# Performance work log

Measured on AMD Instinct MI355X. Metric: run time of the kernel, lower is better.

The kernel has to match this reference:

```python
import jax, jax.numpy as jnp
import numpy as np

B, S, H = 8, 2048, 256
MAX_SEQ = 2048


def get_rotary_matrix(context_window, embedding_dim):
    # Faithful to the llama-from-scratch construction (note the (i-1) quirk):
    # theta_i = 10000 ** (-2*(i-1)/d) for i in [0, d/2)
    half = embedding_dim // 2
    i = jnp.arange(half, dtype=jnp.float32)
    theta = jnp.power(10000.0, -2.0 * (i - 1.0) / embedding_dim)  # [half]
    pos = jnp.arange(context_window, dtype=jnp.float32)  # [S]
    ang = pos[:, None] * theta[None, :]  # [S, half]
    c, s = jnp.cos(ang), jnp.sin(ang)
    R = jnp.zeros((context_window, embedding_dim, embedding_dim), dtype=jnp.float32)
    idx = jnp.arange(half)
    R = R.at[:, 2 * idx, 2 * idx].set(c)
    R = R.at[:, 2 * idx, 2 * idx + 1].set(-s)
    R = R.at[:, 2 * idx + 1, 2 * idx].set(s)
    R = R.at[:, 2 * idx + 1, 2 * idx + 1].set(c)
    return R


def setup_inputs() -> dict:
    key = jax.random.key(0)
    kx, kq, kk, kv = jax.random.split(key, 4)
    scale = 1.0 / np.sqrt(H)
    x = jax.random.normal(kx, (B, S, H), dtype=jnp.float32)
    wq = jax.random.uniform(kq, (H, H), dtype=jnp.float32, minval=-scale, maxval=scale)
    wk = jax.random.uniform(kk, (H, H), dtype=jnp.float32, minval=-scale, maxval=scale)
    wv = jax.random.uniform(kv, (H, H), dtype=jnp.float32, minval=-scale, maxval=scale)
    r = get_rotary_matrix(MAX_SEQ, H)
    return {"x": x, "wq": wq, "wk": wk, "wv": wv, "r": r}


def reference(x, wq, wk, wv, r):
    b, s, h = x.shape
    # nn.Linear(bias=False): y = x @ W.T
    q = jnp.einsum("bsh,oh->bso", x, wq)
    k = jnp.einsum("bsh,oh->bso", x, wk)
    v = jnp.einsum("bsh,oh->bso", x, wv)
    # per-position dense rotary rotation: qr[b,s,:] = q[b,s,:] @ r[s]
    rs = r[:s]
    qr = jnp.einsum("bsh,shk->bsk", q, rs)
    kr = jnp.einsum("bsh,shk->bsk", k, rs)
    attn = jnp.einsum("bqh,bkh->bqk", qr, kr) * (h ** -0.5)  # [B,S,S]
    causal = jnp.tril(jnp.ones((s, s), dtype=bool))
    attn = jnp.where(causal[None, :, :], attn, -jnp.inf)
    attn = jax.nn.softmax(attn, axis=-1)
    out = jnp.einsum("bqk,bkh->bqh", attn, v)
    return out
```

## Files before the change

### kernel.cpp

```cpp
#include <hip/hip_runtime.h>


typedef __bf16 bf16x8 __attribute__((ext_vector_type(8)));
typedef float  f32x4  __attribute__((ext_vector_type(4)));
typedef unsigned short u16x4 __attribute__((ext_vector_type(4)));

#define LOG2E 1.44269504088896340736f
#define LOG2_10000 13.287712379549449f

__device__ __forceinline__ unsigned short f2bf(float f) {
    union { __bf16 h; unsigned short u; } cv;
    cv.h = (__bf16)f;
    return cv.u;
}

__device__ __forceinline__ void gl_lds16(const unsigned short* g, unsigned short* lds) {
    __builtin_amdgcn_global_load_lds(
        (const __attribute__((address_space(1))) unsigned int*)g,
        (__attribute__((address_space(3))) unsigned int*)lds, 16, 0, 0);
}

__global__ __launch_bounds__(256) void prep(
    const float* __restrict__ wq, const float* __restrict__ wk,
    const float* __restrict__ wv,
    float2* __restrict__ cs, unsigned short* __restrict__ wb) {
    int bid = blockIdx.x;
    if (bid < 1024) {
        int id = bid * 256 + threadIdx.x;
        int s = id >> 7;
        int i = id & 127;
        float ex = -2.0f * ((float)i - 1.0f) * (1.0f / 256.0f);
        float theta = exp2f(LOG2_10000 * ex);
        float ang = (float)s * theta;
        float sn, c;
        sincosf(ang, &sn, &c);
        cs[id] = make_float2(c, sn);
    } else {
        int id = (bid - 1024) * 256 + threadIdx.x;
        int sel = id >> 14;
        int off = id & 16383;
        const float* src = (sel == 0) ? wq : (sel == 1) ? wk : wv;
        float4 d = ((const float4*)src)[off];
        u16x4 pk = { f2bf(d.x), f2bf(d.y), f2bf(d.z), f2bf(d.w) };
        *(u16x4*)&wb[(size_t)sel * 65536 + (size_t)off * 4] = pk;
    }
}

__global__ __launch_bounds__(256, 2) void qkv_rope(
    const float* __restrict__ x, const unsigned short* __restrict__ wb,
    const float2* __restrict__ cs,
    unsigned short* __restrict__ qr, unsigned short* __restrict__ kr,
    unsigned short* __restrict__ vt) {

    __shared__ unsigned short Ash[32 * 256];
    __shared__ unsigned short Bsh[256 * 128];

    const int mt  = blockIdx.x;
    const int tid = threadIdx.x;
    const int w = tid >> 6, l = tid & 63;
    const int lane_m = l & 15, quad = l >> 4;
    const int wm = w >> 1, wn = w & 1;

#pragma unroll
    for (int p = 0; p < 8; ++p) {
        int id = p * 256 + tid;
        int row = id >> 6, f4 = id & 63;
        float4 d = *(const float4*)(x + (size_t)(mt * 32 + row) * 256 + f4 * 4);
        u16x4 pk = { f2bf(d.x), f2bf(d.y), f2bf(d.z), f2bf(d.w) };
        int k = f4 * 4;
        int idx = row * 256 + ((((k >> 3) ^ row) << 3) | (k & 7));
        *(u16x4*)&Ash[idx] = pk;
    }

    for (int sel = 0; sel < 3; ++sel) {
        f32x4 acc[8];
#pragma unroll
        for (int c = 0; c < 8; ++c) acc[c] = (f32x4){0.f, 0.f, 0.f, 0.f};

        for (int kc2 = 0; kc2 < 2; ++kc2) {
            __syncthreads();
#pragma unroll
            for (int p = 0; p < 16; ++p) {
                int rb = (p * 4 + w) * 4;
                int rowg = rb + (l >> 4);
                int cg = (l & 15) ^ (rowg & 15);
                gl_lds16(wb + (size_t)sel * 65536 + (size_t)rowg * 256 + kc2 * 128 + cg * 8,
                         &Bsh[rb * 128]);
            }
            __syncthreads();
#pragma unroll
            for (int ks = 0; ks < 4; ++ks) {
                int ck = kc2 * 16 + ks * 4 + quad;
                int cl = ks * 4 + quad;
                int r0 = wm * 16 + lane_m;
                bf16x8 a0 = *(const bf16x8*)&Ash[r0 * 256 + ((ck ^ r0) << 3)];
#pragma unroll
                for (int ct = 0; ct < 8; ++ct) {
                    int nn = wn * 128 + ct * 16 + lane_m;
                    bf16x8 bb = *(const bf16x8*)&Bsh[nn * 128 + (((cl ^ (nn & 15))) << 3)];
                    acc[ct] = __builtin_amdgcn_mfma_f32_16x16x32_bf16(a0, bb, acc[ct], 0, 0, 0);
                }
            }
        }

        int mbase = mt * 32 + wm * 16 + quad * 4;
        if (sel < 2) {
            unsigned short* dst = sel ? kr : qr;
            const float scale = sel ? 1.0f : 0.0625f;
#pragma unroll
            for (int ct = 0; ct < 8; ++ct) {
                int col = wn * 128 + ct * 16 + lane_m;
                int ii = col >> 1;
                float sgn = (col & 1) ? -1.0f : 1.0f;
#pragma unroll
                for (int rr = 0; rr < 4; ++rr) {
                    int m = mbase + rr;
                    int spos = m & 2047;
                    float2 csv = cs[spos * 128 + ii];
                    float v = acc[ct][rr];
                    float pr = __shfl_xor(v, 1);
                    float rot = (csv.x * v + sgn * csv.y * pr) * scale;
                    dst[(size_t)m * 256 + col] = f2bf(rot);
                }
            }
        } else {
#pragma unroll
            for (int ct = 0; ct < 8; ++ct) {
                int col = wn * 128 + ct * 16 + lane_m;
                u16x4 pk = { f2bf(acc[ct][0]), f2bf(acc[ct][1]),
                             f2bf(acc[ct][2]), f2bf(acc[ct][3]) };
                int bb = mbase >> 11;
                int s0 = mbase & 2047;
                *(u16x4*)&vt[((size_t)bb * 256 + col) * 2048 + s0] = pk;
            }
        }
    }
}

__global__ __launch_bounds__(256, 2) void flash_attn(
    const unsigned short* __restrict__ qr, const unsigned short* __restrict__ kr,
    const unsigned short* __restrict__ vt, float* __restrict__ out) {

    __shared__ unsigned short Ksh[64 * 256];
    __shared__ unsigned short Vsh[256 * 64];
    __shared__ unsigned short Psh[32 * 64];

    const int n = blockIdx.x;
    const int b = n & 7;
    const int idx = n >> 3;
    const int j = (idx < 32) ? (63 - idx) : (idx - 32);
    const int q0 = j * 32;

    const int tid = threadIdx.x;
    const int w = tid >> 6, l = tid & 63;
    const int lane_m = l & 15, quad = l >> 4;
    const int qw = w >> 1;
    const int kp = w & 1;

    bf16x8 qf[8];
    {
        const unsigned short* qb =
            qr + ((size_t)(b * 2048 + q0 + qw * 16 + lane_m)) * 256 + quad * 8;
#pragma unroll
        for (int ks = 0; ks < 8; ++ks) qf[ks] = *(const bf16x8*)(qb + ks * 32);
    }

    f32x4 o[16];
#pragma unroll
    for (int t = 0; t < 16; ++t) o[t] = (f32x4){0.f, 0.f, 0.f, 0.f};
    float l_part[4] = {0.f, 0.f, 0.f, 0.f};

    const int nkt = ((q0 + 31) >> 6) + 1;
    const int rmax = q0 + qw * 16 + 15;

#pragma unroll
    for (int p = 0; p < 8; ++p) {
        int rb = (p * 4 + w) * 2;
        int row = rb + (l >> 5);
        int cg = (l & 31) ^ (row & 31);
        gl_lds16(kr + ((size_t)(b * 2048 + row)) * 256 + cg * 8, &Ksh[rb * 256]);
    }
#pragma unroll
    for (int p = 0; p < 8; ++p) {
        int hb = (p * 4 + w) * 8;
        int h = hb + (l >> 3);
        int cg = (l & 7) ^ (h & 7);
        gl_lds16(vt + ((size_t)(b * 256 + h)) * 2048 + cg * 8, &Vsh[hb * 64]);
    }

    for (int kt = 0; kt < nkt; ++kt) {
        const int kv0 = kt * 64;
        const int kv1 = kv0 + 64;
        const bool more = (kt + 1) < nkt;
        __syncthreads();

        const bool active = (kv0 + 32 * kp) <= rmax;
        f32x4 sacc[2];
        if (active) {
#pragma unroll
            for (int ct = 0; ct < 2; ++ct) sacc[ct] = (f32x4){0.f, 0.f, 0.f, 0.f};
#pragma unroll
            for (int ks = 0; ks < 8; ++ks) {
                bf16x8 a = qf[ks];
#pragma unroll
                for (int ct = 0; ct < 2; ++ct) {
                    int kvr = kp * 32 + ct * 16 + lane_m;
                    bf16x8 bb = *(const bf16x8*)&Ksh[kvr * 256 + (((ks * 4 + quad) ^ (kvr & 31)) << 3)];
                    sacc[ct] = __builtin_amdgcn_mfma_f32_16x16x32_bf16(a, bb, sacc[ct], 0, 0, 0);
                }
            }
        }
        __syncthreads();

        if (more) {
#pragma unroll
            for (int p = 0; p < 8; ++p) {
                int rb = (p * 4 + w) * 2;
                int row = rb + (l >> 5);
                int cg = (l & 31) ^ (row & 31);
                gl_lds16(kr + ((size_t)(b * 2048 + kv1 + row)) * 256 + cg * 8, &Ksh[rb * 256]);
            }
        }

        if (active) {
            const bool needmask = (kv0 + kp * 32 + 31) > (q0 + qw * 16);
#pragma unroll
            for (int ct = 0; ct < 2; ++ct) {
                int col_l = kp * 32 + ct * 16 + lane_m;
                int col_g = kv0 + col_l;
#pragma unroll
                for (int rr = 0; rr < 4; ++rr) {
                    float e = exp2f(sacc[ct][rr] * LOG2E);
                    if (needmask) {
                        int row_g = q0 + qw * 16 + quad * 4 + rr;
                        if (col_g > row_g) e = 0.0f;
                    }
                    l_part[rr] += e;
                    int row = qw * 16 + quad * 4 + rr;
                    Psh[row * 64 + ((((col_l >> 3) ^ (row & 7)) << 3) | (col_l & 7))] = f2bf(e);
                }
            }
            {
                int prow = qw * 16 + lane_m;
                int pk = kp * 4 + quad;
                bf16x8 a = *(const bf16x8*)&Psh[prow * 64 + ((pk ^ (prow & 7)) << 3)];
#pragma unroll
                for (int ht = 0; ht < 16; ++ht) {
                    int h = ht * 16 + lane_m;
                    bf16x8 bb = *(const bf16x8*)&Vsh[h * 64 + ((pk ^ (h & 7)) << 3)];
                    o[ht] = __builtin_amdgcn_mfma_f32_16x16x32_bf16(a, bb, o[ht], 0, 0, 0);
                }
            }
        }
        __syncthreads();

        if (more) {
#pragma unroll
            for (int p = 0; p < 8; ++p) {
                int hb = (p * 4 + w) * 8;
                int h = hb + (l >> 3);
                int cg = (l & 7) ^ (h & 7);
                gl_lds16(vt + ((size_t)(b * 256 + h)) * 2048 + kv1 + cg * 8, &Vsh[hb * 64]);
            }
        }
    }

#pragma unroll
    for (int rr = 0; rr < 4; ++rr) {
        l_part[rr] += __shfl_xor(l_part[rr], 1);
        l_part[rr] += __shfl_xor(l_part[rr], 2);
        l_part[rr] += __shfl_xor(l_part[rr], 4);
        l_part[rr] += __shfl_xor(l_part[rr], 8);
    }

    __syncthreads();
    float* mlbuf = (float*)Vsh;
    float* obuf  = (float*)Ksh;
    if (lane_m == 0) {
#pragma unroll
        for (int rr = 0; rr < 4; ++rr)
            mlbuf[(qw * 2 + kp) * 16 + quad * 4 + rr] = l_part[rr];
    }
    if (kp == 1) {
#pragma unroll
        for (int ht = 0; ht < 16; ++ht)
#pragma unroll
            for (int rr = 0; rr < 4; ++rr)
                obuf[(qw * 16 + quad * 4 + rr) * 256 + ht * 16 + lane_m] = o[ht][rr];
    }
    __syncthreads();
    if (kp == 0) {
        float inv[4];
#pragma unroll
        for (int rr = 0; rr < 4; ++rr)
            inv[rr] = 1.0f / (l_part[rr] + mlbuf[(qw * 2 + 1) * 16 + quad * 4 + rr]);
#pragma unroll
        for (int ht = 0; ht < 16; ++ht) {
#pragma unroll
            for (int rr = 0; rr < 4; ++rr) {
                float val = o[ht][rr] +
                            obuf[(qw * 16 + quad * 4 + rr) * 256 + ht * 16 + lane_m];
                size_t idx2 = ((size_t)(b * 2048 + q0 + qw * 16 + quad * 4 + rr)) * 256
                              + ht * 16 + lane_m;
                out[idx2] = val * inv[rr];
            }
        }
    }
}

extern "C" void kernel_launch(void* const* d_in, const int* in_sizes, int n_in,
                              void* d_out, int out_size, void* d_ws, size_t ws_size,
                              hipStream_t stream) {
    const float* x  = (const float*)d_in[0];
    const float* wq = (const float*)d_in[1];
    const float* wk = (const float*)d_in[2];
    const float* wv = (const float*)d_in[3];
    float* out = (float*)d_out;

    char* ws = (char*)d_ws;
    float2*         cs = (float2*)ws;
    unsigned short* qr = (unsigned short*)(ws + (2u << 20));
    unsigned short* kr = (unsigned short*)(ws + (10u << 20));
    unsigned short* vt = (unsigned short*)(ws + (18u << 20));
    unsigned short* wb = (unsigned short*)(ws + (26u << 20));

    prep<<<dim3(1216), dim3(256), 0, stream>>>(wq, wk, wv, cs, wb);
    qkv_rope<<<dim3(512), dim3(256), 0, stream>>>(x, wb, cs, qr, kr, vt);
    flash_attn<<<dim3(512), dim3(256), 0, stream>>>(qr, kr, vt, out);
}
```

Baseline: 650.4 us.

## Double-buffer K/V tiles and repartition attention work across warps

The flash attention kernel now keeps two LDS buffers each for K and V and prefetches tile t+2 while computing tile t, using explicit vmcnt waits and raw barriers. Warp roles change: each warp now computes 16 KV columns of S for all 32 query rows and owns a 64-wide slice of the output head dimension. The old cross-warp reduction of O partials through LDS goes away; only the row sums are combined. Doubling the LDS footprint and moving launch bounds to one block per SM lowers occupancy, which may cost latency hiding.

```diff
diff --git a/kernel.cpp b/kernel.cpp
--- a/kernel.cpp
+++ b/kernel.cpp
@@ -19,6 +19,9 @@
         (const __attribute__((address_space(1))) unsigned int*)g,
         (__attribute__((address_space(3))) unsigned int*)lds, 16, 0, 0);
 }
+
+#define BARRIER_MEMFENCE() asm volatile("s_barrier" ::: "memory")
+#define WAITVM(n) asm volatile("s_waitcnt vmcnt(" #n ")" ::: "memory")
 
 __global__ __launch_bounds__(256) void prep(
     const float* __restrict__ wq, const float* __restrict__ wk,
@@ -137,12 +140,12 @@
     }
 }
 
-__global__ __launch_bounds__(256, 2) void flash_attn(
+__global__ __launch_bounds__(256, 1) void flash_attn(
     const unsigned short* __restrict__ qr, const unsigned short* __restrict__ kr,
     const unsigned short* __restrict__ vt, float* __restrict__ out) {
 
-    __shared__ unsigned short Ksh[64 * 256];
-    __shared__ unsigned short Vsh[256 * 64];
+    __shared__ unsigned short Ksh[2][64 * 256];
+    __shared__ unsigned short Vsh[2][256 * 64];
     __shared__ unsigned short Psh[32 * 64];
 
     const int n = blockIdx.x;
@@ -154,158 +157,147 @@
     const int tid = threadIdx.x;
     const int w = tid >> 6, l = tid & 63;
     const int lane_m = l & 15, quad = l >> 4;
-    const int qw = w >> 1;
-    const int kp = w & 1;
-
-    bf16x8 qf[8];
+
+    bf16x8 qf[2][8];
     {
         const unsigned short* qb =
-            qr + ((size_t)(b * 2048 + q0 + qw * 16 + lane_m)) * 256 + quad * 8;
-#pragma unroll
-        for (int ks = 0; ks < 8; ++ks) qf[ks] = *(const bf16x8*)(qb + ks * 32);
-    }
-
-    f32x4 o[16];
-#pragma unroll
-    for (int t = 0; t < 16; ++t) o[t] = (f32x4){0.f, 0.f, 0.f, 0.f};
-    float l_part[4] = {0.f, 0.f, 0.f, 0.f};
+            qr + ((size_t)(b * 2048 + q0 + lane_m)) * 256 + quad * 8;
+#pragma unroll
+        for (int rt = 0; rt < 2; ++rt)
+#pragma unroll
+            for (int ks = 0; ks < 8; ++ks)
+                qf[rt][ks] = *(const bf16x8*)(qb + rt * 16 * 256 + ks * 32);
+    }
 
     const int nkt = ((q0 + 31) >> 6) + 1;
-    const int rmax = q0 + qw * 16 + 15;
-
-#pragma unroll
-    for (int p = 0; p < 8; ++p) {
-        int rb = (p * 4 + w) * 2;
-        int row = rb + (l >> 5);
-        int cg = (l & 31) ^ (row & 31);
-        gl_lds16(kr + ((size_t)(b * 2048 + row)) * 256 + cg * 8, &Ksh[rb * 256]);
-    }
-#pragma unroll
-    for (int p = 0; p < 8; ++p) {
-        int hb = (p * 4 + w) * 8;
-        int h = hb + (l >> 3);
-        int cg = (l & 7) ^ (h & 7);
-        gl_lds16(vt + ((size_t)(b * 256 + h)) * 2048 + cg * 8, &Vsh[hb * 64]);
-    }
-
-    for (int kt = 0; kt < nkt; ++kt) {
-        const int kv0 = kt * 64;
-        const int kv1 = kv0 + 64;
-        const bool more = (kt + 1) < nkt;
-        __syncthreads();
-
-        const bool active = (kv0 + 32 * kp) <= rmax;
+
+    auto stageK = [&](int kvbase, int buf) {
+#pragma unroll
+        for (int p = 0; p < 8; ++p) {
+            int rb = (p * 4 + w) * 2;
+            int row = rb + (l >> 5);
+            int cg = (l & 31) ^ (row & 31);
+            gl_lds16(kr + ((size_t)(b * 2048 + kvbase + row)) * 256 + cg * 8,
+                     &Ksh[buf][rb * 256]);
+        }
+    };
+    auto stageV = [&](int kvbase, int buf) {
+#pragma unroll
+        for (int p = 0; p < 8; ++p) {
+            int hb = (p * 4 + w) * 8;
+            int h = hb + (l >> 3);
+            int cg = (l & 7) ^ (h & 7);
+            gl_lds16(vt + ((size_t)(b * 256 + h)) * 2048 + kvbase + cg * 8,
+                     &Vsh[buf][hb * 64]);
+        }
+    };
+
+    stageK(0, 0); stageV(0, 0);
+    if (nkt > 1) { stageK(64, 1); stageV(64, 1); }
+    WAITVM(0);
+    BARRIER_MEMFENCE();
+
+    f32x4 o[2][4];
+#pragma unroll
+    for (int rt = 0; rt < 2; ++rt)
+#pragma unroll
+        for (int ht = 0; ht < 4; ++ht) o[rt][ht] = (f32x4){0.f, 0.f, 0.f, 0.f};
+    float l_loc[2][4] = {{0.f, 0.f, 0.f, 0.f}, {0.f, 0.f, 0.f, 0.f}};
+
+    for (int t = 0; t < nkt; ++t) {
+        const int cur = t & 1;
+        const int kv0 = t * 64;
+
         f32x4 sacc[2];
-        if (active) {
-#pragma unroll
-            for (int ct = 0; ct < 2; ++ct) sacc[ct] = (f32x4){0.f, 0.f, 0.f, 0.f};
-#pragma unroll
-            for (int ks = 0; ks < 8; ++ks) {
-                bf16x8 a = qf[ks];
-#pragma unroll
-                for (int ct = 0; ct < 2; ++ct) {
-                    int kvr = kp * 32 + ct * 16 + lane_m;
-                    bf16x8 bb = *(const bf16x8*)&Ksh[kvr * 256 + (((ks * 4 + quad) ^ (kvr & 31)) << 3)];
-                    sacc[ct] = __builtin_amdgcn_mfma_f32_16x16x32_bf16(a, bb, sacc[ct], 0, 0, 0);
-                }
-            }
-        }
-        __syncthreads();
-
-        if (more) {
-#pragma unroll
-            for (int p = 0; p < 8; ++p) {
-                int rb = (p * 4 + w) * 2;
-                int row = rb + (l >> 5);
-                int cg = (l & 31) ^ (row & 31);
-                gl_lds16(kr + ((size_t)(b * 2048 + kv1 + row)) * 256 + cg * 8, &Ksh[rb * 256]);
-            }
-        }
-
-        if (active) {
-            const bool needmask = (kv0 + kp * 32 + 31) > (q0 + qw * 16);
-#pragma unroll
-            for (int ct = 0; ct < 2; ++ct) {
-                int col_l = kp * 32 + ct * 16 + lane_m;
-                int col_g = kv0 + col_l;
-#pragma unroll
-                for (int rr = 0; rr < 4; ++rr) {
-                    float e = exp2f(sacc[ct][rr] * LOG2E);
-                    if (needmask) {
-                        int row_g = q0 + qw * 16 + quad * 4 + rr;
-                        if (col_g > row_g) e = 0.0f;
-                    }
-                    l_part[rr] += e;
-                    int row = qw * 16 + quad * 4 + rr;
-                    Psh[row * 64 + ((((col_l >> 3) ^ (row & 7)) << 3) | (col_l & 7))] = f2bf(e);
-                }
-            }
-            {
-                int prow = qw * 16 + lane_m;
-                int pk = kp * 4 + quad;
-                bf16x8 a = *(const bf16x8*)&Psh[prow * 64 + ((pk ^ (prow & 7)) << 3)];
-#pragma unroll
-                for (int ht = 0; ht < 16; ++ht) {
-                    int h = ht * 16 + lane_m;
-                    bf16x8 bb = *(const bf16x8*)&Vsh[h * 64 + ((pk ^ (h & 7)) << 3)];
-                    o[ht] = __builtin_amdgcn_mfma_f32_16x16x32_bf16(a, bb, o[ht], 0, 0, 0);
-                }
-            }
-        }
-        __syncthreads();
-
-        if (more) {
-#pragma unroll
-            for (int p = 0; p < 8; ++p) {
-                int hb = (p * 4 + w) * 8;
-                int h = hb + (l >> 3);
-                int cg = (l & 7) ^ (h & 7);
-                gl_lds16(vt + ((size_t)(b * 256 + h)) * 2048 + kv1 + cg * 8, &Vsh[hb * 64]);
-            }
-        }
-    }
-
-#pragma unroll
-    for (int rr = 0; rr < 4; ++rr) {
-        l_part[rr] += __shfl_xor(l_part[rr], 1);
-        l_part[rr] += __shfl_xor(l_part[rr], 2);
-        l_part[rr] += __shfl_xor(l_part[rr], 4);
-        l_part[rr] += __shfl_xor(l_part[rr], 8);
-    }
-
+        sacc[0] = (f32x4){0.f, 0.f, 0.f, 0.f};
+        sacc[1] = (f32x4){0.f, 0.f, 0.f, 0.f};
+        const int kvr = w * 16 + lane_m;
+#pragma unroll
+        for (int ks = 0; ks < 8; ++ks) {
+            bf16x8 bb = *(const bf16x8*)
+                &Ksh[cur][kvr * 256 + (((ks * 4 + quad) ^ (kvr & 31)) << 3)];
+            sacc[0] = __builtin_amdgcn_mfma_f32_16x16x32_bf16(qf[0][ks], bb, sacc[0], 0, 0, 0);
+            sacc[1] = __builtin_amdgcn_mfma_f32_16x16x32_bf16(qf[1][ks], bb, sacc[1], 0, 0, 0);
+        }
+
+        const bool needmask = (kv0 + 63) > q0;
+        const int colg = kv0 + w * 16 + lane_m;
+#pragma unroll
+        for (int rt = 0; rt < 2; ++rt) {
+#pragma unroll
+            for (int rr = 0; rr < 4; ++rr) {
+                float e = exp2f(sacc[rt][rr] * LOG2E);
+                if (needmask && colg > (q0 + rt * 16 + quad * 4 + rr)) e = 0.0f;
+                l_loc[rt][rr] += e;
+                int row = rt * 16 + quad * 4 + rr;
+                int col = w * 16 + lane_m;
+                Psh[row * 64 + ((((col >> 3) ^ (row & 7)) << 3) | (col & 7))] = f2bf(e);
+            }
+        }
+        asm volatile("s_waitcnt lgkmcnt(0)" ::: "memory");
+        BARRIER_MEMFENCE();
+
+        if (t + 2 < nkt) stageK(kv0 + 128, cur);
+
+#pragma unroll
+        for (int ks2 = 0; ks2 < 2; ++ks2) {
+            bf16x8 pa[2];
+#pragma unroll
+            for (int rt2 = 0; rt2 < 2; ++rt2) {
+                int prow = rt2 * 16 + lane_m;
+                pa[rt2] = *(const bf16x8*)
+                    &Psh[prow * 64 + (((ks2 * 4 + quad) ^ (prow & 7)) << 3)];
+            }
+#pragma unroll
+            for (int ht = 0; ht < 4; ++ht) {
+                int h = w * 64 + ht * 16 + lane_m;
+                bf16x8 vb = *(const bf16x8*)
+                    &Vsh[cur][h * 64 + (((ks2 * 4 + quad) ^ (h & 7)) << 3)];
+                o[0][ht] = __builtin_amdgcn_mfma_f32_16x16x32_bf16(pa[0], vb, o[0][ht], 0, 0, 0);
+                o[1][ht] = __builtin_amdgcn_mfma_f32_16x16x32_bf16(pa[1], vb, o[1][ht], 0, 0, 0);
+            }
+        }
+        BARRIER_MEMFENCE();
+
+        if (t + 2 < nkt) {
+            stageV(kv0 + 128, cur);
+            WAITVM(16);
+            BARRIER_MEMFENCE();
+        } else if (t + 1 < nkt) {
+            WAITVM(0);
+            BARRIER_MEMFENCE();
+        }
+    }
+
+    WAITVM(0);
     __syncthreads();
-    float* mlbuf = (float*)Vsh;
-    float* obuf  = (float*)Ksh;
-    if (lane_m == 0) {
-#pragma unroll
-        for (int rr = 0; rr < 4; ++rr)
-            mlbuf[(qw * 2 + kp) * 16 + quad * 4 + rr] = l_part[rr];
-    }
-    if (kp == 1) {
-#pragma unroll
-        for (int ht = 0; ht < 16; ++ht)
-#pragma unroll
-            for (int rr = 0; rr < 4; ++rr)
-                obuf[(qw * 16 + quad * 4 + rr) * 256 + ht * 16 + lane_m] = o[ht][rr];
-    }
+    float* lbuf = (float*)Psh;
+#pragma unroll
+    for (int rt = 0; rt < 2; ++rt)
+#pragma unroll
+        for (int rr = 0; rr < 4; ++rr) {
+            float v = l_loc[rt][rr];
+            v += __shfl_xor(v, 1);
+            v += __shfl_xor(v, 2);
+            v += __shfl_xor(v, 4);
+            v += __shfl_xor(v, 8);
+            if (lane_m == 0) lbuf[w * 32 + rt * 16 + quad * 4 + rr] = v;
+        }
     __syncthreads();
-    if (kp == 0) {
-        float inv[4];
-#pragma unroll
-        for (int rr = 0; rr < 4; ++rr)
-            inv[rr] = 1.0f / (l_part[rr] + mlbuf[(qw * 2 + 1) * 16 + quad * 4 + rr]);
-#pragma unroll
-        for (int ht = 0; ht < 16; ++ht) {
-#pragma unroll
-            for (int rr = 0; rr < 4; ++rr) {
-                float val = o[ht][rr] +
-                            obuf[(qw * 16 + quad * 4 + rr) * 256 + ht * 16 + lane_m];
-                size_t idx2 = ((size_t)(b * 2048 + q0 + qw * 16 + quad * 4 + rr)) * 256
-                              + ht * 16 + lane_m;
-                out[idx2] = val * inv[rr];
-            }
-        }
-    }
+#pragma unroll
+    for (int rt = 0; rt < 2; ++rt)
+#pragma unroll
+        for (int rr = 0; rr < 4; ++rr) {
+            int row_l = rt * 16 + quad * 4 + rr;
+            float inv = 1.0f / (lbuf[row_l] + lbuf[32 + row_l] +
+                                lbuf[64 + row_l] + lbuf[96 + row_l]);
+#pragma unroll
+            for (int ht = 0; ht < 4; ++ht) {
+                size_t idx2 = ((size_t)(b * 2048 + q0 + row_l)) * 256
+                              + w * 64 + ht * 16 + lane_m;
+                out[idx2] = o[rt][ht][rr] * inv;
+            }
+        }
 }
 
 extern "C" void kernel_launch(void* const* d_in, const int* in_sizes, int n_in,
```

After: 665.8 us. 1.02x slower.
